# Kernel tuning notes

Hardware: AMD Instinct MI355X
Metric: run time of the kernel (lower is better)

## Reference

```python
import jax, jax.numpy as jnp
import numpy as np

V = 50000
E = 640000
DIM = 128
NUM_EDGE_TYPES = 32


def setup_inputs() -> dict:
    key = jax.random.key(0)
    ks = jax.random.split(key, 8)
    return {
        "node_values": jax.random.normal(ks[0], (V, DIM), dtype=jnp.float32),
        "edge_src": jax.random.randint(ks[1], (E,), 0, V, dtype=jnp.int32),
        "edge_dest": jax.random.randint(ks[2], (E,), 0, V, dtype=jnp.int32),
        "edge_cls": jax.random.randint(ks[3], (E,), 0, NUM_EDGE_TYPES, dtype=jnp.int32),
        "W_src": jax.random.normal(ks[4], (DIM, DIM), dtype=jnp.float32) / np.sqrt(DIM),
        "b_src": jnp.zeros((DIM,), dtype=jnp.float32),
        "W_dest": jax.random.normal(ks[5], (DIM, DIM), dtype=jnp.float32) / np.sqrt(DIM),
        "b_dest": jnp.zeros((DIM,), dtype=jnp.float32),
        "edge_emb": jax.random.normal(ks[6], (NUM_EDGE_TYPES, DIM), dtype=jnp.float32),
    }


def reference(node_values, edge_src, edge_dest, edge_cls, W_src, b_src, W_dest, b_dest, edge_emb):
    # Dense projections over all nodes, then gather per edge (matches tf.gather(dense(...), idx))
    src_proj = node_values @ W_src + b_src    # [V, dim]
    dest_proj = node_values @ W_dest + b_dest  # [V, dim]
    # Per-edge fused message: gather src, gather dest, edge-class embedding lookup, add, relu
    msgs = jax.nn.relu(src_proj[edge_src] + dest_proj[edge_dest] + edge_emb[edge_cls])  # [E, dim]
    # Scatter-reduce messages onto destination nodes
    out = jax.ops.segment_sum(msgs, edge_dest, num_segments=V)  # [V, dim]
    return out
```

## Files before the change

### kernel.cpp

```cpp
#include <hip/hip_runtime.h>


#define V 50000
#define E 640000
#define DIM 128
#define NBIN_F 3125
#define QCAP 384
#define NCHUNK 256
#define EC4 625
#define NPROJ 782
#define NFUSED 1038

typedef __bf16 bf16x8 __attribute__((ext_vector_type(8)));
typedef float  f32x4  __attribute__((ext_vector_type(4)));
typedef float  f32x2  __attribute__((ext_vector_type(2)));

__device__ __forceinline__ float bf2f(unsigned int u16) {
    union { unsigned int i; float f; } c; c.i = u16 << 16; return c.f;
}
__device__ __forceinline__ unsigned int f2bf(float f) {
    union { float f; unsigned int i; } c; c.f = f;
    unsigned int u = c.i;
    return (u + 0x7FFFu + ((u >> 16) & 1u)) >> 16;
}

__global__ __launch_bounds__(256) void mp_setup(
    const float* __restrict__ Ws, const float* __restrict__ Wd,
    const float* __restrict__ emb,
    unsigned short* __restrict__ Wpk, unsigned short* __restrict__ embB,
    int* __restrict__ binCnt)
{
    int tid = blockIdx.x * 256 + threadIdx.x;
    int mat  = tid >> 11;
    int rem  = tid & 2047;
    int ct   = rem >> 8;
    int kt   = (rem >> 6) & 3;
    int lane = rem & 63;
    const float* W = mat ? Wd : Ws;
    int n  = ct * 16 + (lane & 15);
    int k0 = kt * 32 + (lane >> 4) * 8;
    unsigned short* dst = Wpk + (size_t)tid * 8;
    #pragma unroll
    for (int j = 0; j < 8; ++j) dst[j] = (unsigned short)f2bf(W[(k0 + j) * DIM + n]);
    embB[tid] = (unsigned short)f2bf(emb[tid]);
    if (tid < NBIN_F) binCnt[tid] = 0;
}

__global__ __launch_bounds__(256) void mp_fused(
    const int* __restrict__ ed, const int* __restrict__ es, const int* __restrict__ ec,
    int* __restrict__ binCnt, int* __restrict__ binbuf,
    const float* __restrict__ x, const unsigned short* __restrict__ Wpk,
    const float* __restrict__ bs, const float* __restrict__ bd,
    unsigned char* __restrict__ ps8, unsigned short* __restrict__ pdB)
{
    __shared__ float stage[4][16 * 132];

    const int b = blockIdx.x;
    const int t = threadIdx.x;
    const bool isBin = ((b & 3) == 3) && (b < 1024);

    if (isBin) {
        int* cnt = (int*)&stage[0][0];
        const int c = b >> 2;
        for (int i = t; i < NBIN_F; i += 256) cnt[i] = 0;

        int4 DV[3], SV[3], CV[3];
        {
            const int4* ed4 = (const int4*)ed + (size_t)c * EC4;
            const int4* es4 = (const int4*)es + (size_t)c * EC4;
            const int4* ec4 = (const int4*)ec + (size_t)c * EC4;
            #pragma unroll
            for (int k = 0; k < 3; ++k) {
                int i = t + k * 256;
                if (i < EC4) { DV[k] = ed4[i]; SV[k] = es4[i]; CV[k] = ec4[i]; }
                else { DV[k] = make_int4(-1, -1, -1, -1);
                       SV[k] = make_int4(0, 0, 0, 0); CV[k] = make_int4(0, 0, 0, 0); }
            }
        }
        __syncthreads();

        #pragma unroll
        for (int k = 0; k < 3; ++k) {
            #define H1(D) if ((D) >= 0) atomicAdd(&cnt[(unsigned)(D) >> 4], 1);
            H1(DV[k].x); H1(DV[k].y); H1(DV[k].z); H1(DV[k].w);
            #undef H1
        }
        __syncthreads();

        for (int i = t; i < NBIN_F; i += 256) {
            int c0 = cnt[i];
            if (c0) cnt[i] = atomicAdd(&binCnt[i], c0);
        }
        __syncthreads();

        #pragma unroll
        for (int k = 0; k < 3; ++k) {
            #define SC1(D, S, C) if ((D) >= 0) { \
                int bn = (unsigned)(D) >> 4; \
                int sl = atomicAdd(&cnt[bn], 1); \
                if (sl < QCAP) \
                    binbuf[(size_t)bn * QCAP + sl] = \
                        ((S) & 0xFFFF) | ((C) << 16) | (((D) & 15) << 21); }
            SC1(DV[k].x, SV[k].x, CV[k].x); SC1(DV[k].y, SV[k].y, CV[k].y);
            SC1(DV[k].z, SV[k].z, CV[k].z); SC1(DV[k].w, SV[k].w, CV[k].w);
            #undef SC1
        }
        return;
    }

    const int p = b - ((b < 1024) ? ((b + 1) >> 2) : 256);
    if (p >= NPROJ) return;
    const int wave = __builtin_amdgcn_readfirstlane(threadIdx.x) >> 6;
    const int lane = threadIdx.x & 63;
    const int m = lane & 15, q = lane >> 4;
    const int row0 = p * 64 + wave * 16;

    int arow = row0 + m; if (arow >= V) arow = V - 1;
    const float* xr = x + (size_t)arow * DIM + q * 8;

    bf16x8 A[4];
    #pragma unroll
    for (int kt = 0; kt < 4; ++kt) {
        float4 u = *(const float4*)(xr + kt * 32);
        float4 v = *(const float4*)(xr + kt * 32 + 4);
        bf16x8 a;
        a[0] = (__bf16)u.x; a[1] = (__bf16)u.y; a[2] = (__bf16)u.z; a[3] = (__bf16)u.w;
        a[4] = (__bf16)v.x; a[5] = (__bf16)v.y; a[6] = (__bf16)v.z; a[7] = (__bf16)v.w;
        A[kt] = a;
    }

    const bf16x8* Bp = (const bf16x8*)Wpk;

    f32x4 accS[8], accD[8];
    #pragma unroll
    for (int ct = 0; ct < 8; ++ct) {
        f32x4 aS = {0.f, 0.f, 0.f, 0.f}, aD = {0.f, 0.f, 0.f, 0.f};
        #pragma unroll
        for (int kt = 0; kt < 4; ++kt) {
            bf16x8 bS = Bp[((0 * 8 + ct) * 4 + kt) * 64 + lane];
            bf16x8 bD = Bp[((1 * 8 + ct) * 4 + kt) * 64 + lane];
            aS = __builtin_amdgcn_mfma_f32_16x16x32_bf16(A[kt], bS, aS, 0, 0, 0);
            aD = __builtin_amdgcn_mfma_f32_16x16x32_bf16(A[kt], bD, aD, 0, 0, 0);
        }
        accS[ct] = aS; accD[ct] = aD;
    }

    float* st = stage[wave];
    const int rr = lane & 15, cg = lane >> 4;
    const int orow = row0 + rr;
    const float* rowp = st + rr * 132 + cg * 32;

    #pragma unroll
    for (int ct = 0; ct < 8; ++ct) {
        const float bv = bs[ct * 16 + m];
        #pragma unroll
        for (int rg = 0; rg < 4; ++rg)
            st[(q * 4 + rg) * 132 + ct * 16 + m] = accS[ct][rg] + bv;
    }
    __syncthreads();
    {
        int w[8];
        #pragma unroll
        for (int j = 0; j < 8; ++j) {
            float4 f = *(const float4*)(rowp + 4 * j);
            int v = __builtin_amdgcn_cvt_pk_fp8_f32(f.x, f.y, 0, false);
            v = __builtin_amdgcn_cvt_pk_fp8_f32(f.z, f.w, v, true);
            w[j] = v;
        }
        if (orow < V) {
            int4* dst = (int4*)(ps8 + (size_t)orow * 128 + cg * 32);
            dst[0] = make_int4(w[0], w[1], w[2], w[3]);
            dst[1] = make_int4(w[4], w[5], w[6], w[7]);
        }
    }
    __syncthreads();

    #pragma unroll
    for (int ct = 0; ct < 8; ++ct) {
        const float bv = bd[ct * 16 + m];
        #pragma unroll
        for (int rg = 0; rg < 4; ++rg)
            st[(q * 4 + rg) * 132 + ct * 16 + m] = accD[ct][rg] + bv;
    }
    __syncthreads();
    {
        int w[16];
        #pragma unroll
        for (int j = 0; j < 8; ++j) {
            float4 f = *(const float4*)(rowp + 4 * j);
            w[2 * j]     = f2bf(f.x) | (f2bf(f.y) << 16);
            w[2 * j + 1] = f2bf(f.z) | (f2bf(f.w) << 16);
        }
        if (orow < V) {
            int4* dst = (int4*)(pdB + (size_t)orow * 128 + cg * 32);
            #pragma unroll
            for (int jj = 0; jj < 4; ++jj)
                dst[jj] = make_int4(w[4 * jj], w[4 * jj + 1], w[4 * jj + 2], w[4 * jj + 3]);
        }
    }
}

__global__ __launch_bounds__(256) void mp_binBC(
    const unsigned char* __restrict__ ps8, const unsigned short* __restrict__ pdB,
    const unsigned short* __restrict__ embB,
    const int* __restrict__ binCnt, const int* __restrict__ binbuf,
    float* __restrict__ out)
{
    __shared__ int csr[QCAP];
    __shared__ int cnt[16];
    __shared__ int off[17];
    __shared__ int cur[16];
    __shared__ unsigned short sEmb[32 * DIM];

    const int bin = blockIdx.x;
    const int d0 = bin << 4;
    const int t = threadIdx.x;
    const int wave = t >> 6, lane = t & 63;

    int nb = binCnt[bin]; if (nb > QCAP) nb = QCAP;
    const int* buf = binbuf + (size_t)bin * QCAP;

    if (t < 16) cnt[t] = 0;

    {
        const int4* s4 = (const int4*)embB;
        int4* d4 = (int4*)sEmb;
        d4[t] = s4[t];
        d4[t + 256] = s4[t + 256];
    }

    int EB[2];
    EB[0] = (t < nb) ? buf[t] : -1;
    EB[1] = (t + 256 < nb) ? buf[t + 256] : -1;

    float dp0v[4], dp1v[4];
    #pragma unroll
    for (int k = 0; k < 4; ++k) {
        int d = d0 + wave + k * 4;
        unsigned int pdu = *(const unsigned int*)(pdB + (size_t)d * DIM + 2 * lane);
        dp0v[k] = bf2f(pdu & 0xFFFF); dp1v[k] = bf2f(pdu >> 16);
    }
    __syncthreads();

    #pragma unroll
    for (int k = 0; k < 2; ++k) {
        unsigned int rl = (unsigned)EB[k] >> 21;
        if (rl < 16u) atomicAdd(&cnt[rl], 1);
    }
    __syncthreads();

    if (t < 16) {
        int v = cnt[t];
        #pragma unroll
        for (int dlt = 1; dlt < 16; dlt <<= 1) {
            int u = __shfl_up(v, dlt, 64);
            if (t >= dlt) v += u;
        }
        off[t + 1] = v;
        cur[t] = v - cnt[t];
        if (t == 0) off[0] = 0;
    }
    __syncthreads();

    #pragma unroll
    for (int k = 0; k < 2; ++k) {
        unsigned int rl = (unsigned)EB[k] >> 21;
        if (rl < 16u) {
            int pos = atomicAdd(&cur[rl], 1);
            csr[pos] = EB[k];
        }
    }
    __syncthreads();

    #define PROC(P) { \
        int s_ = *(const unsigned short*)(ps8 + ((size_t)((P) & 0xFFFF) << 7) + 2 * lane); \
        unsigned int e_ = *(const unsigned int*)(sEmb + ((((P) >> 16) & 0x1F) << 7) + 2 * lane); \
        f32x2 f_ = __builtin_amdgcn_cvt_pk_f32_fp8(s_, false); \
        a0 += fmaxf(f_.x + dp0 + bf2f(e_ & 0xFFFF), 0.f); \
        a1 += fmaxf(f_.y + dp1 + bf2f(e_ >> 16),    0.f); }

    #pragma unroll
    for (int k = 0; k < 4; ++k) {
        const int rl = wave + k * 4;
        const int d = d0 + rl;
        int i0 = off[rl], i1 = off[rl + 1];
        const float dp0 = dp0v[k], dp1 = dp1v[k];
        float a0 = 0.f, a1 = 0.f;
        int i = i0;
        for (; i + 8 <= i1; i += 8) {
            int p0 = csr[i],     p1 = csr[i + 1], p2 = csr[i + 2], p3 = csr[i + 3];
            int p4 = csr[i + 4], p5 = csr[i + 5], p6 = csr[i + 6], p7 = csr[i + 7];
            PROC(p0); PROC(p1); PROC(p2); PROC(p3);
            PROC(p4); PROC(p5); PROC(p6); PROC(p7);
        }
        for (; i + 4 <= i1; i += 4) {
            int p0 = csr[i], p1 = csr[i + 1], p2 = csr[i + 2], p3 = csr[i + 3];
            PROC(p0); PROC(p1); PROC(p2); PROC(p3);
        }
        for (; i < i1; ++i) { int p0 = csr[i]; PROC(p0); }
        *(float2*)(out + (size_t)d * DIM + 2 * lane) = make_float2(a0, a1);
    }
    #undef PROC
}

extern "C" void kernel_launch(void* const* d_in, const int* in_sizes, int n_in,
                              void* d_out, int out_size, void* d_ws, size_t ws_size,
                              hipStream_t stream) {
    const float* x   = (const float*)d_in[0];
    const int*   es  = (const int*)d_in[1];
    const int*   ed  = (const int*)d_in[2];
    const int*   ec  = (const int*)d_in[3];
    const float* Ws  = (const float*)d_in[4];
    const float* bs  = (const float*)d_in[5];
    const float* Wd  = (const float*)d_in[6];
    const float* bd  = (const float*)d_in[7];
    const float* emb = (const float*)d_in[8];
    float* out = (float*)d_out;

    char* ws = (char*)d_ws;
    size_t off = 0;
    unsigned char*  ps8  = (unsigned char*)(ws + off);  off += (size_t)V * 128;
    unsigned short* pdB  = (unsigned short*)(ws + off); off += (size_t)V * DIM * 2;
    int* binbuf = (int*)(ws + off);                     off += (size_t)NBIN_F * QCAP * 4;
    int* binCnt = (int*)(ws + off);                     off += (size_t)NBIN_F * 4;
    unsigned short* Wpk  = (unsigned short*)(ws + off); off += 2 * 128 * 128 * 2;
    unsigned short* embB = (unsigned short*)(ws + off); off += 32 * 128 * 2;

    mp_setup<<<16, 256, 0, stream>>>(Ws, Wd, emb, Wpk, embB, binCnt);
    mp_fused<<<NFUSED, 256, 0, stream>>>(ed, es, ec, binCnt, binbuf,
                                         x, Wpk, bs, bd, ps8, pdB);
    mp_binBC<<<NBIN_F, 256, 0, stream>>>(ps8, pdB, embB, binCnt, binbuf, out);
}
```

Baseline: 158.6 us.

## Replace LDS-aggregated binning blocks with per-edge global atomic scatter blocks

The binning phase changes from 256 large blocks, which built LDS histograms and reserved bin ranges with one global atomic per bin, to 2500 small blocks that each handle 256 edges, with one global atomicAdd per edge. Scatter blocks are interleaved 3:1 with projection blocks, and the grid grows to 3336 blocks. The aim is more parallelism and shorter per-block latency, so binning overlaps better with the projection GEMM. The cost is 640k contended global atomics on about 3125 bin counters in place of LDS aggregation.

```diff
diff --git a/kernel.cpp b/kernel.cpp
--- a/kernel.cpp
+++ b/kernel.cpp
@@ -6,10 +6,9 @@
 #define DIM 128
 #define NBIN_F 3125
 #define QCAP 384
-#define NCHUNK 256
-#define EC4 625
+#define NSCAT 2500
 #define NPROJ 782
-#define NFUSED 1038
+#define NFUSED 3336
 
 typedef __bf16 bf16x8 __attribute__((ext_vector_type(8)));
 typedef float  f32x4  __attribute__((ext_vector_type(4)));
@@ -57,58 +56,22 @@
 
     const int b = blockIdx.x;
     const int t = threadIdx.x;
-    const bool isBin = ((b & 3) == 3) && (b < 1024);
-
-    if (isBin) {
-        int* cnt = (int*)&stage[0][0];
-        const int c = b >> 2;
-        for (int i = t; i < NBIN_F; i += 256) cnt[i] = 0;
-
-        int4 DV[3], SV[3], CV[3];
-        {
-            const int4* ed4 = (const int4*)ed + (size_t)c * EC4;
-            const int4* es4 = (const int4*)es + (size_t)c * EC4;
-            const int4* ec4 = (const int4*)ec + (size_t)c * EC4;
-            #pragma unroll
-            for (int k = 0; k < 3; ++k) {
-                int i = t + k * 256;
-                if (i < EC4) { DV[k] = ed4[i]; SV[k] = es4[i]; CV[k] = ec4[i]; }
-                else { DV[k] = make_int4(-1, -1, -1, -1);
-                       SV[k] = make_int4(0, 0, 0, 0); CV[k] = make_int4(0, 0, 0, 0); }
-            }
-        }
-        __syncthreads();
-
-        #pragma unroll
-        for (int k = 0; k < 3; ++k) {
-            #define H1(D) if ((D) >= 0) atomicAdd(&cnt[(unsigned)(D) >> 4], 1);
-            H1(DV[k].x); H1(DV[k].y); H1(DV[k].z); H1(DV[k].w);
-            #undef H1
-        }
-        __syncthreads();
-
-        for (int i = t; i < NBIN_F; i += 256) {
-            int c0 = cnt[i];
-            if (c0) cnt[i] = atomicAdd(&binCnt[i], c0);
-        }
-        __syncthreads();
-
-        #pragma unroll
-        for (int k = 0; k < 3; ++k) {
-            #define SC1(D, S, C) if ((D) >= 0) { \
-                int bn = (unsigned)(D) >> 4; \
-                int sl = atomicAdd(&cnt[bn], 1); \
-                if (sl < QCAP) \
-                    binbuf[(size_t)bn * QCAP + sl] = \
-                        ((S) & 0xFFFF) | ((C) << 16) | (((D) & 15) << 21); }
-            SC1(DV[k].x, SV[k].x, CV[k].x); SC1(DV[k].y, SV[k].y, CV[k].y);
-            SC1(DV[k].z, SV[k].z, CV[k].z); SC1(DV[k].w, SV[k].w, CV[k].w);
-            #undef SC1
-        }
+
+    if ((b & 3) != 0) {
+        const int s = b - (b >> 2) - 1;
+        if (s >= NSCAT) return;
+        const int i = s * 256 + t;
+        const int d  = ed[i];
+        const int sr = es[i];
+        const int cl = ec[i];
+        const int bn = (unsigned)d >> 4;
+        const int val = (sr & 0xFFFF) | (cl << 16) | ((d & 15) << 21);
+        const int pos = atomicAdd(&binCnt[bn], 1);
+        if (pos < QCAP) binbuf[(size_t)bn * QCAP + pos] = val;
         return;
     }
 
-    const int p = b - ((b < 1024) ? ((b + 1) >> 2) : 256);
+    const int p = b >> 2;
     if (p >= NPROJ) return;
     const int wave = __builtin_amdgcn_readfirstlane(threadIdx.x) >> 6;
     const int lane = threadIdx.x & 63;
```

New measurement: 190.3 us. +20.0%, slower.
